# Kernel tuning notes

Hardware: AMD Instinct MI355X
Metric: run time of the kernel (lower is better)

The kernel has to match this reference:

```python
import jax, jax.numpy as jnp
import numpy as np

NUM_JOINTS = 21
BN_EPS = 1e-5


def hand_adjacency():
    J = NUM_JOINTS
    a = np.zeros((J, J), dtype=np.float32)
    # wrist to finger bases
    for j in (1, 5, 9, 13, 17):
        a[0, j] = a[j, 0] = 1
    # finger chains
    for base in (1, 5, 9, 13, 17):
        for i in range(base, base + 3):
            a[i, i + 1] = a[i + 1, i] = 1
    a += np.eye(J, dtype=np.float32)
    d = a.sum(axis=1)
    dinv = np.power(d, -0.5)
    dinv[np.isinf(dinv)] = 0.0
    D = np.diag(dinv)
    return (D @ a @ D).astype(np.float32)


def setup_inputs() -> dict:
    key = jax.random.key(0)
    ks = jax.random.split(key, 16)
    S, B, HD = 256, 128, 42
    IN, HID = 2, 64
    x = jax.random.normal(ks[0], (S, B, HD), dtype=jnp.float32)
    # xavier-uniform weights
    lim1 = float(np.sqrt(6.0 / (IN + HID)))
    lim2 = float(np.sqrt(6.0 / (HID + IN)))
    W1 = jax.random.uniform(ks[1], (IN, HID), minval=-lim1, maxval=lim1, dtype=jnp.float32)
    b1 = jnp.zeros((HID,), dtype=jnp.float32)
    W2 = jax.random.uniform(ks[2], (HID, IN), minval=-lim2, maxval=lim2, dtype=jnp.float32)
    b2 = jnp.zeros((IN,), dtype=jnp.float32)
    # BatchNorm (eval mode): affine params + running stats
    g1 = 1.0 + 0.1 * jax.random.normal(ks[3], (HID,), dtype=jnp.float32)
    be1 = 0.1 * jax.random.normal(ks[4], (HID,), dtype=jnp.float32)
    m1 = 0.1 * jax.random.normal(ks[5], (HID,), dtype=jnp.float32)
    v1 = 0.5 + jax.random.uniform(ks[6], (HID,), dtype=jnp.float32)
    g2 = 1.0 + 0.1 * jax.random.normal(ks[7], (IN,), dtype=jnp.float32)
    be2 = 0.1 * jax.random.normal(ks[8], (IN,), dtype=jnp.float32)
    m2 = 0.1 * jax.random.normal(ks[9], (IN,), dtype=jnp.float32)
    v2 = 0.5 + jax.random.uniform(ks[10], (IN,), dtype=jnp.float32)
    adj = jnp.asarray(hand_adjacency())
    return {"x": x, "adj": adj, "W1": W1, "b1": b1, "W2": W2, "b2": b2,
            "g1": g1, "be1": be1, "m1": m1, "v1": v1,
            "g2": g2, "be2": be2, "m2": m2, "v2": v2}


def _gcn_bn(h, adj, W, b, g, be, m, v, act):
    # h: (S, B, J, Cin) -> (S, B, J, Cout)
    s = jnp.einsum('sbjc,cd->sbjd', h, W)          # feature transform
    o = jnp.einsum('ij,sbjd->sbid', adj, s) + b    # joint aggregation + bias
    o = (o - m) * (g * jax.lax.rsqrt(v + BN_EPS)) + be  # BN eval, per-channel
    return jax.nn.relu(o) if act else o


def reference(x, adj, W1, b1, W2, b2, g1, be1, m1, v1, g2, be2, m2, v2):
    S, B, HD = x.shape
    C = HD // NUM_JOINTS
    h = x.reshape(S, B, NUM_JOINTS, C)
    h = _gcn_bn(h, adj, W1, b1, g1, be1, m1, v1, act=True)   # dropout is identity in eval
    h = _gcn_bn(h, adj, W2, b2, g2, be2, m2, v2, act=False)
    return h.reshape(S, B, HD) + x
```

## Files before the change

### kernel.cpp

```cpp
#include <hip/hip_runtime.h>

typedef float f2 __attribute__((ext_vector_type(2)));

#define NJ 21

#define W00 0.16666667f
#define W0B 0.23570226f
#define W33 0.33333333f
#define WMT 0.40824829f
#define WTT 0.5f

template<int PAT>
__device__ __forceinline__ float dpp_add(float v) {
    int r = __builtin_amdgcn_update_dpp(0, __float_as_int(v), PAT, 0xF, 0xF, true);
    return v + __int_as_float(r);
}

__device__ __forceinline__ void aggregate(const f2* __restrict__ s, f2* __restrict__ d) {
    d[0] = W00 * s[0] + W0B * (s[1] + s[5] + s[9] + s[13] + s[17]);
#pragma unroll
    for (int f = 1; f <= 17; f += 4) {
        d[f]     = W0B * s[0] + W33 * (s[f] + s[f + 1]);
        d[f + 1] = W33 * (s[f] + s[f + 1] + s[f + 2]);
        d[f + 2] = W33 * (s[f + 1] + s[f + 2]) + WMT * s[f + 3];
        d[f + 3] = WMT * s[f + 2] + WTT * s[f + 3];
    }
}

__global__ __launch_bounds__(256) void hgcn_kernel(
    const float* __restrict__ x,
    const float* __restrict__ adj,
    const float* __restrict__ W1,
    const float* __restrict__ b1,
    const float* __restrict__ W2,
    const float* __restrict__ b2,
    const float* __restrict__ g1,
    const float* __restrict__ be1,
    const float* __restrict__ m1,
    const float* __restrict__ v1,
    const float* __restrict__ g2,
    const float* __restrict__ be2,
    const float* __restrict__ m2,
    const float* __restrict__ v2,
    float* __restrict__ out)
{
    (void)adj;
    __shared__ float4 sc1[4][68];
    __shared__ float  sc2[4][68];

    const int tid = threadIdx.x;
    const int wv  = tid >> 6;
    const int ln  = tid & 63;
    const int tl  = ln >> 2;
    const int q   = ln & 3;

    const size_t tok = (size_t)blockIdx.x * 64 + (size_t)wv * 16 + tl;
    const float* __restrict__ xt = x + tok * 42;

    f2 h[NJ];
#pragma unroll
    for (int j = 0; j < NJ; ++j) {
        const float2 t = ((const float2*)xt)[j];
        h[j] = (f2){t.x, t.y};
    }

    const float k20 = g2[0] * rsqrtf(v2[0] + 1e-5f);
    const float k21 = g2[1] * rsqrtf(v2[1] + 1e-5f);
    const float D0  = (b2[0] - m2[0]) * k20 + be2[0];
    const float D1  = (b2[1] - m2[1]) * k21 + be2[1];
    {
        const int d = ln;
        const float k1   = g1[d] * rsqrtf(v1[d] + 1e-5f);
        const float2 w2d = *(const float2*)(W2 + 2 * d);
        const int idx = d + (d >> 4);
        sc1[wv][idx] = make_float4(W1[d] * k1, W1[64 + d] * k1,
                                   (b1[d] - m1[d]) * k1 + be1[d], w2d.x * k20);
        sc2[wv][idx] = w2d.y * k21;
    }
    __builtin_amdgcn_wave_barrier();
    __builtin_amdgcn_sched_barrier(0);

    f2 a[NJ + 1];
    aggregate(h, a);
    a[NJ] = (f2){0.f, 0.f};

    f2 ap0[11], ap1[11];
#pragma unroll
    for (int k = 0; k < 11; ++k) {
        ap0[k] = (f2){a[2 * k].x, a[2 * k + 1].x};
        ap1[k] = (f2){a[2 * k].y, a[2 * k + 1].y};
    }

    f2 s0[11], s1[11];
#pragma unroll
    for (int k = 0; k < 11; ++k) { s0[k] = (f2){0.f, 0.f}; s1[k] = (f2){0.f, 0.f}; }

    const float4* __restrict__ c1w = (const float4*)sc1[wv];
    const float*  __restrict__ c2w = sc2[wv];
    const int cbase = q * 17;
#pragma unroll
    for (int dd = 0; dd < 16; ++dd) {
        const float4 c  = c1w[cbase + dd];
        const float w21 = c2w[cbase + dd];
#pragma unroll
        for (int k = 0; k < 11; ++k) {
            f2 v = ap0[k] * c.x + ap1[k] * c.y + c.z;
            v = __builtin_elementwise_max(v, (f2){0.f, 0.f});
            s0[k] += v * c.w;
            s1[k] += v * w21;
        }
    }

#pragma unroll
    for (int k = 0; k < 11; ++k) {
        s0[k].x = dpp_add<0xB1>(s0[k].x);  s0[k].x = dpp_add<0x4E>(s0[k].x);
        s0[k].y = dpp_add<0xB1>(s0[k].y);  s0[k].y = dpp_add<0x4E>(s0[k].y);
        s1[k].x = dpp_add<0xB1>(s1[k].x);  s1[k].x = dpp_add<0x4E>(s1[k].x);
        s1[k].y = dpp_add<0xB1>(s1[k].y);  s1[k].y = dpp_add<0x4E>(s1[k].y);
    }

    f2 vv[NJ], o[NJ];
#pragma unroll
    for (int j = 0; j < NJ; ++j) {
        vv[j].x = (j & 1) ? s0[j >> 1].y : s0[j >> 1].x;
        vv[j].y = (j & 1) ? s1[j >> 1].y : s1[j >> 1].x;
    }
    aggregate(vv, o);

    float* __restrict__ og = out + tok * 42;
#pragma unroll
    for (int j = 0; j < NJ; ++j) {
        if ((j & 3) == q) {
            float2 st;
            st.x = o[j].x + h[j].x + D0;
            st.y = o[j].y + h[j].y + D1;
            ((float2*)og)[j] = st;
        }
    }
}

extern "C" void kernel_launch(void* const* d_in, const int* in_sizes, int n_in,
                              void* d_out, int out_size, void* d_ws, size_t ws_size,
                              hipStream_t stream) {
    (void)in_sizes; (void)n_in; (void)d_ws; (void)ws_size; (void)out_size;
    const float* x   = (const float*)d_in[0];
    const float* adj = (const float*)d_in[1];
    const float* W1  = (const float*)d_in[2];
    const float* b1  = (const float*)d_in[3];
    const float* W2  = (const float*)d_in[4];
    const float* b2  = (const float*)d_in[5];
    const float* g1  = (const float*)d_in[6];
    const float* be1 = (const float*)d_in[7];
    const float* m1  = (const float*)d_in[8];
    const float* v1  = (const float*)d_in[9];
    const float* g2  = (const float*)d_in[10];
    const float* be2 = (const float*)d_in[11];
    const float* m2  = (const float*)d_in[12];
    const float* v2  = (const float*)d_in[13];

    hgcn_kernel<<<512, 256, 0, stream>>>(x, adj, W1, b1, W2, b2,
                                         g1, be1, m1, v1, g2, be2, m2, v2,
                                         (float*)d_out);
}
```

Measured before the change: 89.04 us.

## Split each token's hidden channels across eight lanes instead of four

Each token is now handled by 8 lanes, each covering 8 hidden channels, rather than 4 lanes covering 16. This halves the per-lane inner loop, adds a third DPP reduction step, and doubles the grid to 1024 blocks, with launch bounds set for 4 blocks per CU. The residual values are reloaded per lane so the full h array need not stay live until the end, easing register pressure. The cost is more duplicated aggregation work and more redundant x loads per token.

```diff
diff --git a/kernel.cpp b/kernel.cpp
--- a/kernel.cpp
+++ b/kernel.cpp
@@ -10,9 +10,9 @@
 #define WMT 0.40824829f
 #define WTT 0.5f
 
-template<int PAT>
+template<int CTRL>
 __device__ __forceinline__ float dpp_add(float v) {
-    int r = __builtin_amdgcn_update_dpp(0, __float_as_int(v), PAT, 0xF, 0xF, true);
+    int r = __builtin_amdgcn_update_dpp(0, __float_as_int(v), CTRL, 0xF, 0xF, true);
     return v + __int_as_float(r);
 }
 
@@ -27,7 +27,7 @@
     }
 }
 
-__global__ __launch_bounds__(256) void hgcn_kernel(
+__global__ __launch_bounds__(256, 4) void hgcn_kernel(
     const float* __restrict__ x,
     const float* __restrict__ adj,
     const float* __restrict__ W1,
@@ -51,10 +51,10 @@
     const int tid = threadIdx.x;
     const int wv  = tid >> 6;
     const int ln  = tid & 63;
-    const int tl  = ln >> 2;
-    const int q   = ln & 3;
+    const int tl  = ln >> 3;
+    const int li  = ln & 7;
 
-    const size_t tok = (size_t)blockIdx.x * 64 + (size_t)wv * 16 + tl;
+    const size_t tok = (size_t)blockIdx.x * 32 + (size_t)wv * 8 + tl;
     const float* __restrict__ xt = x + tok * 42;
 
     f2 h[NJ];
@@ -62,6 +62,17 @@
     for (int j = 0; j < NJ; ++j) {
         const float2 t = ((const float2*)xt)[j];
         h[j] = (f2){t.x, t.y};
+    }
+
+    f2 rh[3];
+    rh[0] = (f2){0.f, 0.f}; rh[1] = (f2){0.f, 0.f}; rh[2] = (f2){0.f, 0.f};
+#pragma unroll
+    for (int r = 0; r < 3; ++r) {
+        const int j = li + 8 * r;
+        if (j < NJ) {
+            const float2 t = ((const float2*)xt)[j];
+            rh[r] = (f2){t.x, t.y};
+        }
     }
 
     const float k20 = g2[0] * rsqrtf(v2[0] + 1e-5f);
@@ -97,11 +108,12 @@
 
     const float4* __restrict__ c1w = (const float4*)sc1[wv];
     const float*  __restrict__ c2w = sc2[wv];
-    const int cbase = q * 17;
 #pragma unroll
-    for (int dd = 0; dd < 16; ++dd) {
-        const float4 c  = c1w[cbase + dd];
-        const float w21 = c2w[cbase + dd];
+    for (int dd = 0; dd < 8; ++dd) {
+        const int   dg  = li * 8 + dd;
+        const int   idx = dg + (dg >> 4);
+        const float4 c  = c1w[idx];
+        const float w21 = c2w[idx];
 #pragma unroll
         for (int k = 0; k < 11; ++k) {
             f2 v = ap0[k] * c.x + ap1[k] * c.y + c.z;
@@ -113,10 +125,10 @@
 
 #pragma unroll
     for (int k = 0; k < 11; ++k) {
-        s0[k].x = dpp_add<0xB1>(s0[k].x);  s0[k].x = dpp_add<0x4E>(s0[k].x);
-        s0[k].y = dpp_add<0xB1>(s0[k].y);  s0[k].y = dpp_add<0x4E>(s0[k].y);
-        s1[k].x = dpp_add<0xB1>(s1[k].x);  s1[k].x = dpp_add<0x4E>(s1[k].x);
-        s1[k].y = dpp_add<0xB1>(s1[k].y);  s1[k].y = dpp_add<0x4E>(s1[k].y);
+        s0[k].x = dpp_add<0xB1>(s0[k].x); s0[k].x = dpp_add<0x4E>(s0[k].x); s0[k].x = dpp_add<0x141>(s0[k].x);
+        s0[k].y = dpp_add<0xB1>(s0[k].y); s0[k].y = dpp_add<0x4E>(s0[k].y); s0[k].y = dpp_add<0x141>(s0[k].y);
+        s1[k].x = dpp_add<0xB1>(s1[k].x); s1[k].x = dpp_add<0x4E>(s1[k].x); s1[k].x = dpp_add<0x141>(s1[k].x);
+        s1[k].y = dpp_add<0xB1>(s1[k].y); s1[k].y = dpp_add<0x4E>(s1[k].y); s1[k].y = dpp_add<0x141>(s1[k].y);
     }
 
     f2 vv[NJ], o[NJ];
@@ -130,10 +142,10 @@
     float* __restrict__ og = out + tok * 42;
 #pragma unroll
     for (int j = 0; j < NJ; ++j) {
-        if ((j & 3) == q) {
+        if ((j & 7) == li) {
             float2 st;
-            st.x = o[j].x + h[j].x + D0;
-            st.y = o[j].y + h[j].y + D1;
+            st.x = o[j].x + rh[j >> 3].x + D0;
+            st.y = o[j].y + rh[j >> 3].y + D1;
             ((float2*)og)[j] = st;
         }
     }
@@ -158,7 +170,7 @@
     const float* m2  = (const float*)d_in[12];
     const float* v2  = (const float*)d_in[13];
 
-    hgcn_kernel<<<512, 256, 0, stream>>>(x, adj, W1, b1, W2, b2,
-                                         g1, be1, m1, v1, g2, be2, m2, v2,
-                                         (float*)d_out);
+    hgcn_kernel<<<1024, 256, 0, stream>>>(x, adj, W1, b1, W2, b2,
+                                          g1, be1, m1, v1, g2, be2, m2, v2,
+                                          (float*)d_out);
 }
```

After: 97.62 us. +9.6%, slower.
